# Kernel tuning notes

Measured on AMD Instinct MI355X. Metric: run time of the kernel, lower is better.

The kernel has to match this reference:

```python
import jax, jax.numpy as jnp
import numpy as np

N_HEADS = 16


def setup_inputs() -> dict:
    key = jax.random.key(0)
    ks = jax.random.split(key, 5)
    B, S, D = 2, 2048, 1024
    scale = 1.0 / np.sqrt(D)
    return {
        "x": jax.random.normal(ks[0], (B, S, D), dtype=jnp.float32),
        "w_in": jax.random.normal(ks[1], (3 * D, D), dtype=jnp.float32) * scale,
        "b_in": jax.random.normal(ks[2], (3 * D,), dtype=jnp.float32) * 0.01,
        "w_out": jax.random.normal(ks[3], (D, D), dtype=jnp.float32) * scale,
        "b_out": jax.random.normal(ks[4], (D,), dtype=jnp.float32) * 0.01,
        "mask": 1,
    }


def reference(x, w_in, b_in, w_out, b_out, mask):
    b, s, d = x.shape
    h = N_HEADS
    dh = d // h
    # fused QKV projection (torch Linear: x @ W^T + b)
    qkv = jnp.einsum("bsd,ed->bse", x, w_in) + b_in  # [b, s, 3d]
    q, k, v = jnp.split(qkv, 3, axis=-1)
    # [b, s, d] -> [b, h, s, dh]
    q = q.reshape(b, s, h, dh).transpose(0, 2, 1, 3)
    k = k.reshape(b, s, h, dh).transpose(0, 2, 1, 3)
    v = v.reshape(b, s, h, dh).transpose(0, 2, 1, 3)
    att = jnp.einsum("bhqd,bhkd->bhqk", q, k)
    if mask:
        causal = jnp.triu(jnp.ones((s, s), dtype=bool), k=1)
        att = jnp.where(causal, -jnp.inf, att)
    att = att / jnp.sqrt(jnp.asarray(dh, att.dtype))
    att = jax.nn.softmax(att, axis=-1)
    out = jnp.einsum("bhqk,bhkd->bhqd", att, v)  # [b, h, s, dh]
    out = out.transpose(0, 2, 1, 3).reshape(b, s, d)
    return jnp.einsum("bsd,ed->bse", out, w_out) + b_out
```

## Files before the change

kernel.cpp:

```cpp
#include <hip/hip_runtime.h>
#include <hip/hip_bf16.h>
#include <cmath>

typedef __hip_bfloat16 bf16;
typedef short v8s __attribute__((ext_vector_type(8)));
typedef short v4s __attribute__((ext_vector_type(4)));
typedef float v4f __attribute__((ext_vector_type(4)));

#define AS1(p) ((__attribute__((address_space(1))) void*)(p))
#define AS3(p) ((__attribute__((address_space(3))) void*)(p))

__device__ __forceinline__ v4f mfma_bf16(v8s a, v8s b, v4f c) {
    return __builtin_amdgcn_mfma_f32_16x16x32_bf16(a, b, c, 0, 0, 0);
}

__device__ __forceinline__ short bf16_bits(float f) {
    return __builtin_bit_cast(short, __float2bfloat16(f));
}

__global__ __launch_bounds__(256)
void cvt_all(const float* __restrict__ x, const float* __restrict__ w_in,
             const float* __restrict__ w_out, bf16* __restrict__ xb,
             bf16* __restrict__ wib, bf16* __restrict__ wob)
{
    const int i = blockIdx.x * 256 + threadIdx.x;
    const float* src; bf16* dst; int j;
    if (i < 1048576)      { src = x;     dst = xb;  j = i; }
    else if (i < 1835008) { src = w_in;  dst = wib; j = i - 1048576; }
    else                  { src = w_out; dst = wob; j = i - 1835008; }
    const float4 v = ((const float4*)src)[j];
    v4s p;
    p.x = bf16_bits(v.x); p.y = bf16_bits(v.y);
    p.z = bf16_bits(v.z); p.w = bf16_bits(v.w);
    ((v4s*)dst)[j] = p;
}

template<int NF>
__global__ __launch_bounds__(256)
void gemm_bt(const bf16* __restrict__ A, const bf16* __restrict__ Bt,
             const float* __restrict__ bias, bf16* __restrict__ C,
             float* __restrict__ Cf, int N, int K, int lda)
{
    constexpr int BN = NF * 32;
    __shared__ __align__(16) bf16 As[2][128 * 32];
    __shared__ __align__(16) bf16 Bs[2][BN * 32];

    const int t    = threadIdx.x;
    const int lane = t & 63;
    const int wave = t >> 6;
    const int l16  = lane & 15;
    const int quad = lane >> 4;
    const int m0   = blockIdx.y * 128;
    const int n0   = blockIdx.x * BN;
    const int wm   = (wave >> 1) * 64;
    const int wn   = (wave & 1) * (NF * 16);

    const v4f zf = {0.f, 0.f, 0.f, 0.f};
    v4f acc[4][NF];
#pragma unroll
    for (int i = 0; i < 4; ++i)
#pragma unroll
        for (int j = 0; j < NF; ++j) acc[i][j] = zf;

    const int sr = t >> 2;
    const int g  = ((t & 3) ^ ((sr >> 1) & 3)) * 8;
    const bf16* gA = A  + (size_t)(m0 + sr) * lda + g;
    const bf16* gB = Bt + (size_t)(n0 + sr) * K + g;

    auto stage = [&](int kt, int buf) {
        const int k0 = kt * 32;
        char* lA = (char*)&As[buf][0] + t * 16;
        char* lB = (char*)&Bs[buf][0] + t * 16;
        __builtin_amdgcn_global_load_lds(AS1(gA + k0),                    AS3(lA),        16, 0, 0);
        __builtin_amdgcn_global_load_lds(AS1(gA + (size_t)64 * lda + k0), AS3(lA + 4096), 16, 0, 0);
        __builtin_amdgcn_global_load_lds(AS1(gB + k0),                    AS3(lB),        16, 0, 0);
        if (NF == 4)
            __builtin_amdgcn_global_load_lds(AS1(gB + (size_t)64 * K + k0), AS3(lB + 4096), 16, 0, 0);
    };

    stage(0, 0);
    const int KT = K >> 5;
    const int xs = ((l16 >> 1) & 3) * 8;
    for (int kt = 0; kt < KT; ++kt) {
        const int buf = kt & 1;
        __syncthreads();
        if (kt + 1 < KT) stage(kt + 1, buf ^ 1);

        v8s af[4], bfr[NF];
#pragma unroll
        for (int mi = 0; mi < 4; ++mi)
            af[mi] = *(const v8s*)(&As[buf][0] + (wm + mi * 16 + l16) * 32
                                   + ((quad * 8) ^ xs));
#pragma unroll
        for (int ni = 0; ni < NF; ++ni)
            bfr[ni] = *(const v8s*)(&Bs[buf][0] + (wn + ni * 16 + l16) * 32
                                    + ((quad * 8) ^ xs));
#pragma unroll
        for (int mi = 0; mi < 4; ++mi)
#pragma unroll
            for (int ni = 0; ni < NF; ++ni)
                acc[mi][ni] = mfma_bf16(af[mi], bfr[ni], acc[mi][ni]);
    }

#pragma unroll
    for (int ni = 0; ni < NF; ++ni) {
        const int col = n0 + wn + ni * 16 + l16;
        const float bv = bias[col];
#pragma unroll
        for (int mi = 0; mi < 4; ++mi) {
#pragma unroll
            for (int r = 0; r < 4; ++r) {
                const int row = m0 + wm + mi * 16 + quad * 4 + r;
                const float fv = acc[mi][ni][r] + bv;
                if (Cf) Cf[(size_t)row * N + col] = fv;
                else    C [(size_t)row * N + col] = __float2bfloat16(fv);
            }
        }
    }
}

__global__ __launch_bounds__(256)
void vtrans(const bf16* __restrict__ qkv, bf16* __restrict__ Vt)
{
    __shared__ short Ts[64][72];
    const int t  = threadIdx.x;
    const int st = blockIdx.x;
    const int bh = blockIdx.y;
    const int b = bh >> 4, h = bh & 15;
    const int s0 = st * 64;
    {
        const int i = t >> 2, j0 = (t & 3) * 16;
        const bf16* src = qkv + (size_t)(b * 2048 + s0 + i) * 3072 + 2048 + h * 64 + j0;
        const v8s a0 = *(const v8s*)(src);
        const v8s a1 = *(const v8s*)(src + 8);
        *(v8s*)&Ts[i][j0]     = a0;
        *(v8s*)&Ts[i][j0 + 8] = a1;
    }
    __syncthreads();
    {
        const int d = t >> 2, seg = (t & 3) * 16;
        v8s o0, o1;
#pragma unroll
        for (int m = 0; m < 8; ++m) { o0[m] = Ts[seg + m][d]; o1[m] = Ts[seg + 8 + m][d]; }
        bf16* dst = Vt + (size_t)(bh * 64 + d) * 2048 + s0 + seg;
        *(v8s*)dst       = o0;
        *(v8s*)(dst + 8) = o1;
    }
}

#define M_STATIC 14.0f
__global__ __launch_bounds__(256)
void attn(bf16* __restrict__ qkv, const bf16* __restrict__ Vt)
{
    __shared__ __align__(16) bf16 Ks[2][64 * 64];
    __shared__ __align__(16) bf16 Vs[2][64 * 64];
    __shared__ __align__(16) short Ps[4][16 * 72];

    const int t    = threadIdx.x;
    const int lane = t & 63;
    const int w    = t >> 6;
    const int l16  = lane & 15;
    const int quad = lane >> 4;
    const int id   = blockIdx.x;
    const int bh   = id & 31;
    const int qb   = 31 - (id >> 5);
    const int b = bh >> 4, h = bh & 15;
    const int T = qb + 1;
    const int rowq = qb * 64 + w * 16;

    v8s qf[2];
    {
        const bf16* Qb = qkv + (size_t)(b * 2048 + rowq + l16) * 3072 + h * 64 + quad * 8;
        qf[0] = *(const v8s*)(Qb);
        qf[1] = *(const v8s*)(Qb + 32);
    }

    const int sr  = t >> 3;
    const int swz = ((t & 7) ^ (sr & 7)) * 8;
    const bf16* kbase = qkv + (size_t)(b * 2048 + sr) * 3072 + 1024 + h * 64 + swz;
    const bf16* vbase = Vt + (size_t)(bh * 64 + sr) * 2048 + swz;
    char* kd = (char*)&Ks[0][0] + t * 16;
    char* vd = (char*)&Vs[0][0] + t * 16;

    __builtin_amdgcn_global_load_lds(AS1(kbase),                     AS3(kd),        16, 0, 0);
    __builtin_amdgcn_global_load_lds(AS1(kbase + (size_t)32 * 3072), AS3(kd + 4096), 16, 0, 0);
    __builtin_amdgcn_global_load_lds(AS1(vbase),                     AS3(vd),        16, 0, 0);
    __builtin_amdgcn_global_load_lds(AS1(vbase + (size_t)32 * 2048), AS3(vd + 4096), 16, 0, 0);

    const v4f zf = {0.f, 0.f, 0.f, 0.f};
    v4f o[4] = {zf, zf, zf, zf};
    float lsum[4] = {0.f, 0.f, 0.f, 0.f};
    short* Pw = &Ps[w][0];
    const int xsw = (l16 & 7) * 8;

    for (int tile = 0; tile < T; ++tile) {
        const int buf = tile & 1;
        __syncthreads();
        if (tile + 1 < T) {
            const int nb = buf ^ 1;
            const bf16* ksrc = kbase + (size_t)((tile + 1) * 64) * 3072;
            const bf16* vsrc = vbase + (tile + 1) * 64;
            char* kdn = (char*)&Ks[nb][0] + t * 16;
            char* vdn = (char*)&Vs[nb][0] + t * 16;
            __builtin_amdgcn_global_load_lds(AS1(ksrc),                     AS3(kdn),        16, 0, 0);
            __builtin_amdgcn_global_load_lds(AS1(ksrc + (size_t)32 * 3072), AS3(kdn + 4096), 16, 0, 0);
            __builtin_amdgcn_global_load_lds(AS1(vsrc),                     AS3(vdn),        16, 0, 0);
            __builtin_amdgcn_global_load_lds(AS1(vsrc + (size_t)32 * 2048), AS3(vdn + 4096), 16, 0, 0);
        }

        v4f s[4] = {zf, zf, zf, zf};
#pragma unroll
        for (int ks = 0; ks < 2; ++ks)
#pragma unroll
            for (int ct = 0; ct < 4; ++ct) {
                const v8s kf = *(const v8s*)(&Ks[buf][0] + (ct * 16 + l16) * 64
                                             + (((ks * 4 + quad) * 8) ^ xsw));
                s[ct] = mfma_bf16(qf[ks], kf, s[ct]);
            }

        if (tile == T - 1) {
            const int colb = tile * 64;
            const int rowb = rowq + quad * 4;
#pragma unroll
            for (int ct = 0; ct < 4; ++ct) {
                const int col = colb + ct * 16 + l16;
#pragma unroll
                for (int r = 0; r < 4; ++r) {
                    const float p = (col > rowb + r)
                        ? 0.f : __expf(fmaf(s[ct][r], 0.125f, -M_STATIC));
                    lsum[r] += p;
                    Pw[(quad * 4 + r) * 72 + ct * 16 + l16] = bf16_bits(p);
                }
            }
        } else {
#pragma unroll
            for (int ct = 0; ct < 4; ++ct)
#pragma unroll
                for (int r = 0; r < 4; ++r) {
                    const float p = __expf(fmaf(s[ct][r], 0.125f, -M_STATIC));
                    lsum[r] += p;
                    Pw[(quad * 4 + r) * 72 + ct * 16 + l16] = bf16_bits(p);
                }
        }
        asm volatile("s_waitcnt lgkmcnt(0)" ::: "memory");

#pragma unroll
        for (int ks = 0; ks < 2; ++ks) {
            const v8s pf = *(const v8s*)(Pw + l16 * 72 + ks * 32 + quad * 8);
#pragma unroll
            for (int nt = 0; nt < 4; ++nt) {
                const v8s vf = *(const v8s*)(&Vs[buf][0] + (nt * 16 + l16) * 64
                                             + (((ks * 4 + quad) * 8) ^ xsw));
                o[nt] = mfma_bf16(pf, vf, o[nt]);
            }
        }
    }

#pragma unroll
    for (int r = 0; r < 4; ++r) {
        float l = lsum[r];
        l += __shfl_xor(l, 1); l += __shfl_xor(l, 2);
        l += __shfl_xor(l, 4); l += __shfl_xor(l, 8);
        lsum[r] = fmaxf(l, 1e-30f);
    }

#pragma unroll
    for (int nt = 0; nt < 4; ++nt)
#pragma unroll
        for (int r = 0; r < 4; ++r) {
            const int row = rowq + quad * 4 + r;
            qkv[(size_t)(b * 2048 + row) * 3072 + 2048 + h * 64 + nt * 16 + l16] =
                __float2bfloat16(o[nt][r] / lsum[r]);
        }
}

extern "C" void kernel_launch(void* const* d_in, const int* in_sizes, int n_in,
                              void* d_out, int out_size, void* d_ws, size_t ws_size,
                              hipStream_t stream)
{
    (void)in_sizes; (void)n_in; (void)out_size; (void)ws_size;
    const float* x     = (const float*)d_in[0];
    const float* w_in  = (const float*)d_in[1];
    const float* b_in  = (const float*)d_in[2];
    const float* w_out = (const float*)d_in[3];
    const float* b_out = (const float*)d_in[4];
    float* out = (float*)d_out;

    bf16* ws     = (bf16*)d_ws;
    bf16* xb     = ws;
    bf16* w_inb  = xb     + (size_t)4096 * 1024;
    bf16* w_outb = w_inb  + (size_t)3072 * 1024;
    bf16* qkv    = w_outb + (size_t)1024 * 1024;
    bf16* vt     = (bf16*)d_out;

    cvt_all<<<8192, 256, 0, stream>>>(x, w_in, w_out, xb, w_inb, w_outb);

    gemm_bt<4><<<dim3(24, 32), dim3(256), 0, stream>>>(xb, w_inb, b_in, qkv, nullptr,
                                                       3072, 1024, 1024);
    vtrans<<<dim3(32, 32), dim3(256), 0, stream>>>(qkv, vt);
    attn<<<1024, 256, 0, stream>>>(qkv, vt);
    gemm_bt<2><<<dim3(16, 32), dim3(256), 0, stream>>>(qkv + 2048, w_outb, b_out, nullptr,
                                                       out, 1024, 1024, 3072);
}
```

Before: 188.2 us.

## Fuse V transpose into QKV GEMM epilogue and load V fragments from global

The QKV GEMM epilogue now writes the V columns straight into a head-major transposed Vt buffer, so the separate vtrans kernel and its extra pass over V are gone. Q/K go into a narrower 2048-wide buffer and attention output goes to its own buffer. In attention, V is no longer staged through LDS; each lane reads its MFMA V fragments directly from global memory, which saves LDS space and async copies. The cost is scattered 2-byte stores with poor coalescing in the GEMM epilogue and uncached global V reads issued inside the attention loop, which may add latency.

```diff
diff --git a/kernel.cpp b/kernel.cpp
--- a/kernel.cpp
+++ b/kernel.cpp
@@ -39,7 +39,8 @@
 __global__ __launch_bounds__(256)
 void gemm_bt(const bf16* __restrict__ A, const bf16* __restrict__ Bt,
              const float* __restrict__ bias, bf16* __restrict__ C,
-             float* __restrict__ Cf, int N, int K, int lda)
+             float* __restrict__ Cf, bf16* __restrict__ Vt,
+             int K, int lda, int ldc)
 {
     constexpr int BN = NF * 32;
     __shared__ __align__(16) bf16 As[2][128 * 32];
@@ -112,48 +113,27 @@
             for (int r = 0; r < 4; ++r) {
                 const int row = m0 + wm + mi * 16 + quad * 4 + r;
                 const float fv = acc[mi][ni][r] + bv;
-                if (Cf) Cf[(size_t)row * N + col] = fv;
-                else    C [(size_t)row * N + col] = __float2bfloat16(fv);
+                if (Vt && col >= 2048) {
+                    const int e = col - 2048;
+                    const int hh = e >> 6, d = e & 63;
+                    const int bb = row >> 11, s = row & 2047;
+                    Vt[((((size_t)(bb * 16 + hh)) * 64 + d) << 11) + s] = __float2bfloat16(fv);
+                } else if (Cf) {
+                    Cf[(size_t)row * ldc + col] = fv;
+                } else {
+                    C[(size_t)row * ldc + col] = __float2bfloat16(fv);
+                }
             }
         }
-    }
-}
-
-__global__ __launch_bounds__(256)
-void vtrans(const bf16* __restrict__ qkv, bf16* __restrict__ Vt)
-{
-    __shared__ short Ts[64][72];
-    const int t  = threadIdx.x;
-    const int st = blockIdx.x;
-    const int bh = blockIdx.y;
-    const int b = bh >> 4, h = bh & 15;
-    const int s0 = st * 64;
-    {
-        const int i = t >> 2, j0 = (t & 3) * 16;
-        const bf16* src = qkv + (size_t)(b * 2048 + s0 + i) * 3072 + 2048 + h * 64 + j0;
-        const v8s a0 = *(const v8s*)(src);
-        const v8s a1 = *(const v8s*)(src + 8);
-        *(v8s*)&Ts[i][j0]     = a0;
-        *(v8s*)&Ts[i][j0 + 8] = a1;
-    }
-    __syncthreads();
-    {
-        const int d = t >> 2, seg = (t & 3) * 16;
-        v8s o0, o1;
-#pragma unroll
-        for (int m = 0; m < 8; ++m) { o0[m] = Ts[seg + m][d]; o1[m] = Ts[seg + 8 + m][d]; }
-        bf16* dst = Vt + (size_t)(bh * 64 + d) * 2048 + s0 + seg;
-        *(v8s*)dst       = o0;
-        *(v8s*)(dst + 8) = o1;
     }
 }
 
 #define M_STATIC 14.0f
 __global__ __launch_bounds__(256)
-void attn(bf16* __restrict__ qkv, const bf16* __restrict__ Vt)
+void attn(const bf16* __restrict__ qkv, const bf16* __restrict__ Vt,
+          bf16* __restrict__ att)
 {
     __shared__ __align__(16) bf16 Ks[2][64 * 64];
-    __shared__ __align__(16) bf16 Vs[2][64 * 64];
     __shared__ __align__(16) short Ps[4][16 * 72];
 
     const int t    = threadIdx.x;
@@ -170,22 +150,23 @@
 
     v8s qf[2];
     {
-        const bf16* Qb = qkv + (size_t)(b * 2048 + rowq + l16) * 3072 + h * 64 + quad * 8;
+        const bf16* Qb = qkv + (size_t)(b * 2048 + rowq + l16) * 2048 + h * 64 + quad * 8;
         qf[0] = *(const v8s*)(Qb);
         qf[1] = *(const v8s*)(Qb + 32);
     }
 
     const int sr  = t >> 3;
     const int swz = ((t & 7) ^ (sr & 7)) * 8;
-    const bf16* kbase = qkv + (size_t)(b * 2048 + sr) * 3072 + 1024 + h * 64 + swz;
-    const bf16* vbase = Vt + (size_t)(bh * 64 + sr) * 2048 + swz;
+    const bf16* kbase = qkv + (size_t)(b * 2048 + sr) * 2048 + 1024 + h * 64 + swz;
     char* kd = (char*)&Ks[0][0] + t * 16;
-    char* vd = (char*)&Vs[0][0] + t * 16;
+
+    const bf16* vrow[4];
+#pragma unroll
+    for (int nt = 0; nt < 4; ++nt)
+        vrow[nt] = Vt + (size_t)(bh * 64 + nt * 16 + l16) * 2048 + quad * 8;
 
     __builtin_amdgcn_global_load_lds(AS1(kbase),                     AS3(kd),        16, 0, 0);
-    __builtin_amdgcn_global_load_lds(AS1(kbase + (size_t)32 * 3072), AS3(kd + 4096), 16, 0, 0);
-    __builtin_amdgcn_global_load_lds(AS1(vbase),                     AS3(vd),        16, 0, 0);
-    __builtin_amdgcn_global_load_lds(AS1(vbase + (size_t)32 * 2048), AS3(vd + 4096), 16, 0, 0);
+    __builtin_amdgcn_global_load_lds(AS1(kbase + (size_t)32 * 2048), AS3(kd + 4096), 16, 0, 0);
 
     const v4f zf = {0.f, 0.f, 0.f, 0.f};
     v4f o[4] = {zf, zf, zf, zf};
@@ -197,16 +178,18 @@
         const int buf = tile & 1;
         __syncthreads();
         if (tile + 1 < T) {
-            const int nb = buf ^ 1;
-            const bf16* ksrc = kbase + (size_t)((tile + 1) * 64) * 3072;
-            const bf16* vsrc = vbase + (tile + 1) * 64;
-            char* kdn = (char*)&Ks[nb][0] + t * 16;
-            char* vdn = (char*)&Vs[nb][0] + t * 16;
+            const bf16* ksrc = kbase + (size_t)((tile + 1) * 64) * 2048;
+            char* kdn = (char*)&Ks[buf ^ 1][0] + t * 16;
             __builtin_amdgcn_global_load_lds(AS1(ksrc),                     AS3(kdn),        16, 0, 0);
-            __builtin_amdgcn_global_load_lds(AS1(ksrc + (size_t)32 * 3072), AS3(kdn + 4096), 16, 0, 0);
-            __builtin_amdgcn_global_load_lds(AS1(vsrc),                     AS3(vdn),        16, 0, 0);
-            __builtin_amdgcn_global_load_lds(AS1(vsrc + (size_t)32 * 2048), AS3(vdn + 4096), 16, 0, 0);
-        }
+            __builtin_amdgcn_global_load_lds(AS1(ksrc + (size_t)32 * 2048), AS3(kdn + 4096), 16, 0, 0);
+        }
+
+        v8s vfr[2][4];
+#pragma unroll
+        for (int ks = 0; ks < 2; ++ks)
+#pragma unroll
+            for (int nt = 0; nt < 4; ++nt)
+                vfr[ks][nt] = *(const v8s*)(vrow[nt] + tile * 64 + ks * 32);
 
         v4f s[4] = {zf, zf, zf, zf};
 #pragma unroll
@@ -248,11 +231,8 @@
         for (int ks = 0; ks < 2; ++ks) {
             const v8s pf = *(const v8s*)(Pw + l16 * 72 + ks * 32 + quad * 8);
 #pragma unroll
-            for (int nt = 0; nt < 4; ++nt) {
-                const v8s vf = *(const v8s*)(&Vs[buf][0] + (nt * 16 + l16) * 64
-                                             + (((ks * 4 + quad) * 8) ^ xsw));
-                o[nt] = mfma_bf16(pf, vf, o[nt]);
-            }
+            for (int nt = 0; nt < 4; ++nt)
+                o[nt] = mfma_bf16(pf, vfr[ks][nt], o[nt]);
         }
     }
 
@@ -269,7 +249,7 @@
 #pragma unroll
         for (int r = 0; r < 4; ++r) {
             const int row = rowq + quad * 4 + r;
-            qkv[(size_t)(b * 2048 + row) * 3072 + 2048 + h * 64 + nt * 16 + l16] =
+            att[(size_t)(b * 2048 + row) * 1024 + h * 64 + nt * 16 + l16] =
                 __float2bfloat16(o[nt][r] / lsum[r]);
         }
 }
@@ -291,14 +271,14 @@
     bf16* w_inb  = xb     + (size_t)4096 * 1024;
     bf16* w_outb = w_inb  + (size_t)3072 * 1024;
     bf16* qkv    = w_outb + (size_t)1024 * 1024;
+    bf16* att    = qkv    + (size_t)4096 * 2048;
     bf16* vt     = (bf16*)d_out;
 
     cvt_all<<<8192, 256, 0, stream>>>(x, w_in, w_out, xb, w_inb, w_outb);
 
     gemm_bt<4><<<dim3(24, 32), dim3(256), 0, stream>>>(xb, w_inb, b_in, qkv, nullptr,
-                                                       3072, 1024, 1024);
-    vtrans<<<dim3(32, 32), dim3(256), 0, stream>>>(qkv, vt);
-    attn<<<1024, 256, 0, stream>>>(qkv, vt);
-    gemm_bt<2><<<dim3(16, 32), dim3(256), 0, stream>>>(qkv + 2048, w_outb, b_out, nullptr,
-                                                       out, 1024, 1024, 3072);
-}
+                                                       vt, 1024, 1024, 2048);
+    attn<<<1024, 256, 0, stream>>>(qkv, vt, att);
+    gemm_bt<2><<<dim3(16, 32), dim3(256), 0, stream>>>(att, w_outb, b_out, nullptr,
+                                                       out, nullptr, 1024, 1024, 1024);
+}
```

Result: slower. 228.2 us (+21.3%).
